# Kernel tuning notes

Hardware: AMD Instinct MI355X
Metric: run time of the kernel (lower is better)

## Reference

```python
import jax, jax.numpy as jnp
import numpy as np
import math

D_MODEL = 1024
NUM_HEADS = 16
MAX_LEN = 2048
B, S = 2, 2048


def setup_inputs() -> dict:
    key = jax.random.key(0)
    ks = jax.random.split(key, 6)
    w_scale = 1.0 / math.sqrt(D_MODEL)  # ~xavier
    return {
        "x": jax.random.normal(ks[0], (B, S, D_MODEL), dtype=jnp.float32),
        "Wq": jax.random.normal(ks[1], (D_MODEL, D_MODEL), dtype=jnp.float32) * w_scale,
        "bq": jnp.zeros((D_MODEL,), dtype=jnp.float32),
        "Wk": jax.random.normal(ks[2], (D_MODEL, D_MODEL), dtype=jnp.float32) * w_scale,
        "bk": jnp.zeros((D_MODEL,), dtype=jnp.float32),
        "Wv": jax.random.normal(ks[3], (D_MODEL, D_MODEL), dtype=jnp.float32) * w_scale,
        "bv": jnp.zeros((D_MODEL,), dtype=jnp.float32),
        "Wo": jax.random.normal(ks[4], (D_MODEL, D_MODEL), dtype=jnp.float32) * w_scale,
        "bo": jnp.zeros((D_MODEL,), dtype=jnp.float32),
        "Er": jax.random.normal(ks[5], (MAX_LEN, D_MODEL // NUM_HEADS), dtype=jnp.float32),
    }


def reference(x, Wq, bq, Wk, bk, Wv, bv, Wo, bo, Er):
    Bsz, Sl, Dm = x.shape
    H = NUM_HEADS
    dqk = Dm // H

    def split_heads(z):
        # [B,S,D] -> [B,H,S,dqk]
        return z.reshape(Bsz, Sl, H, dqk).transpose(0, 2, 1, 3)

    Q = split_heads(x @ Wq.T + bq)
    K = split_heads(x @ Wk.T + bk)
    V = split_heads(x @ Wv.T + bv)

    Er_sl = Er[MAX_LEN - Sl:, :]  # [S, dqk]
    # Faithful to source: contract over d -> [B,H,S], unsqueeze last dim
    QEr = jnp.einsum('bhld,ld->bhl', Q, Er_sl)[..., None]  # [B,H,S,1]
    # skew(): pad left by 1 on last dim, reshape, drop first row
    padded = jnp.pad(QEr, ((0, 0), (0, 0), (0, 0), (1, 0)))  # [B,H,S,2]
    Srel = padded.reshape(Bsz, H, 2, Sl)[:, :, 1:, :]  # [B,H,1,S]

    QK_t = jnp.einsum('bhld,bhmd->bhlm', Q, K)  # [B,H,S,S]
    attn_scores = (QK_t + Srel) / math.sqrt(dqk)

    causal = jnp.tril(jnp.ones((Sl, Sl), dtype=bool))  # [S,S]
    attn_scores = jnp.where(causal[None, None], attn_scores, -jnp.inf)

    attn_probs = jax.nn.softmax(attn_scores, axis=-1)
    attn_out = jnp.einsum('bhlm,bhmd->bhld', attn_probs, V)  # [B,H,S,dqk]
    attn_out = attn_out.transpose(0, 2, 1, 3).reshape(Bsz, Sl, Dm)
    return attn_out @ Wo.T + bo  # dropout omitted (eval mode)
```

## Files before the change

### kernel.cpp

```cpp
#include <hip/hip_runtime.h>
#include <hip/hip_bf16.h>

#define D_MODEL 1024
#define NHEAD 16
#define DH 64
#define BSZ 2
#define SEQ 2048
#define MROWS (BSZ*SEQ)
#define SCL_Q 0.1803368801111204f
#define CHSZ2 16896

typedef __attribute__((ext_vector_type(4))) float f32x4;
typedef __attribute__((ext_vector_type(8))) __bf16 bf16x8;
typedef __attribute__((ext_vector_type(8))) unsigned short u16x8;

__device__ __forceinline__ float b2f(unsigned short u) {
    union { unsigned int i; float f; } v; v.i = ((unsigned int)u) << 16; return v.f;
}
__device__ __forceinline__ unsigned short f2b(float f) {
    union { float f; unsigned int i; } v; v.f = f;
    unsigned int u = v.i;
    u += 0x7fffu + ((u >> 16) & 1u);
    return (unsigned short)(u >> 16);
}

__device__ __forceinline__ char* slotptr(char* wsb, int s) {
    const size_t MB = 1024*1024;
    if (s < 372)  return wsb + 8*MB            + (size_t)s * CHSZ2;
    if (s < 868)  return wsb + 32*MB           + (size_t)(s - 372) * CHSZ2;
    return              wsb + 48*MB + 262144   + (size_t)(s - 868) * CHSZ2;
}

#define GLDS16(gptr, lptr) \
    __builtin_amdgcn_global_load_lds((__attribute__((address_space(1))) void*)(gptr), \
                                     (__attribute__((address_space(3))) void*)(lptr), 16, 0, 0)

__global__ __launch_bounds__(256) void cvt5(
    const float* __restrict__ sx,
    const float* __restrict__ s1, const float* __restrict__ s2,
    const float* __restrict__ s3, const float* __restrict__ s4,
    unsigned short* __restrict__ dx,
    unsigned short* __restrict__ d1, unsigned short* __restrict__ d2,
    unsigned short* __restrict__ d3, unsigned short* __restrict__ d4)
{
    const int seg = blockIdx.y;
    const float* src; unsigned short* dst; int n4;
    if (seg == 0)      { src = sx; dst = dx; n4 = MROWS*D_MODEL/4; }
    else if (seg == 1) { src = s1; dst = d1; n4 = D_MODEL*D_MODEL/4; }
    else if (seg == 2) { src = s2; dst = d2; n4 = D_MODEL*D_MODEL/4; }
    else if (seg == 3) { src = s3; dst = d3; n4 = D_MODEL*D_MODEL/4; }
    else               { src = s4; dst = d4; n4 = D_MODEL*D_MODEL/4; }
    int i = blockIdx.x * 256 + threadIdx.x;
    int stride = gridDim.x * 256;
    for (; i < n4; i += stride) {
        float4 v = ((const float4*)src)[i];
        ushort4 o;
        o.x = f2b(v.x); o.y = f2b(v.y); o.z = f2b(v.z); o.w = f2b(v.w);
        ((ushort4*)dst)[i] = o;
    }
}

__global__ __launch_bounds__(256) void gemm_qkv(
    const unsigned short* __restrict__ X,
    const unsigned short* __restrict__ Wq, const unsigned short* __restrict__ Wk,
    const unsigned short* __restrict__ Wv,
    const float* __restrict__ bq, const float* __restrict__ bk, const float* __restrict__ bv,
    unsigned short* __restrict__ Qo, unsigned short* __restrict__ Ko, unsigned short* __restrict__ Vo)
{
    __shared__ unsigned short lsA[2][128*32];
    __shared__ unsigned short lsB[2][128*32];
    const int tid = threadIdx.x;
    const int z = blockIdx.z;
    const unsigned short* W = (z==0) ? Wq : (z==1) ? Wk : Wv;
    const float* bias = (z==0) ? bq : (z==1) ? bk : bv;
    unsigned short* Out = (z==0) ? Qo : (z==1) ? Ko : Vo;
    const int tM = blockIdx.y * 128;
    const int tN = blockIdx.x * 128;
    const int w = tid >> 6, lane = tid & 63;
    const int wr = w >> 1, wc = w & 1;
    const int lr = lane & 15, lk = lane >> 4;
    const f32x4 fz = {0.f, 0.f, 0.f, 0.f};
    f32x4 acc[4][4];
    #pragma unroll
    for (int m = 0; m < 4; m++)
        #pragma unroll
        for (int n = 0; n < 4; n++) acc[m][n] = fz;

    const int e0 = tid, e1 = 256 + tid;
    const int r0 = e0 >> 2, c0 = ((e0 & 3) ^ (r0 & 3)) * 8;
    const int r1 = e1 >> 2, c1 = ((e1 & 3) ^ (r1 & 3)) * 8;

#define GEMM_STAGE(buf, k0_) do { \
        GLDS16(X + (size_t)(tM + r0) * D_MODEL + (k0_) + c0, &lsA[buf][e0 * 8]); \
        GLDS16(X + (size_t)(tM + r1) * D_MODEL + (k0_) + c1, &lsA[buf][e1 * 8]); \
        GLDS16(W + (size_t)(tN + r0) * D_MODEL + (k0_) + c0, &lsB[buf][e0 * 8]); \
        GLDS16(W + (size_t)(tN + r1) * D_MODEL + (k0_) + c1, &lsB[buf][e1 * 8]); \
    } while (0)

    GEMM_STAGE(0, 0);
    __syncthreads();
    int cur = 0;
    for (int k0 = 0; k0 < D_MODEL; k0 += 32) {
        if (k0 + 32 < D_MODEL) GEMM_STAGE(cur ^ 1, k0 + 32);
        bf16x8 af[4], bfr[4];
        #pragma unroll
        for (int m = 0; m < 4; m++) {
            int row = wr*64 + m*16 + lr;
            af[m] = *(const bf16x8*)&lsA[cur][row*32 + ((lk ^ (row & 3)) * 8)];
        }
        #pragma unroll
        for (int n = 0; n < 4; n++) {
            int row = wc*64 + n*16 + lr;
            bfr[n] = *(const bf16x8*)&lsB[cur][row*32 + ((lk ^ (row & 3)) * 8)];
        }
        #pragma unroll
        for (int m = 0; m < 4; m++)
            #pragma unroll
            for (int n = 0; n < 4; n++)
                acc[m][n] = __builtin_amdgcn_mfma_f32_16x16x32_bf16(af[m], bfr[n], acc[m][n], 0, 0, 0);
        __syncthreads();
        cur ^= 1;
    }
#undef GEMM_STAGE
    const float qscl = (z == 0) ? SCL_Q : 1.0f;
    #pragma unroll
    for (int m = 0; m < 4; m++) {
        int ibase = tM + wr*64 + m*16 + lk*4;
        #pragma unroll
        for (int n = 0; n < 4; n++) {
            int j = tN + wc*64 + n*16 + lr;
            float bj = bias[j];
            int h = j >> 6, d = j & 63;
            #pragma unroll
            for (int r = 0; r < 4; r++) {
                int row = ibase + r;
                int b = row >> 11, s = row & 2047;
                Out[((size_t)(b*NHEAD + h) * SEQ + s) * DH + d] = f2b((acc[m][n][r] + bj) * qscl);
            }
        }
    }
}

__global__ __launch_bounds__(512) void gemm_out(
    const unsigned short* __restrict__ X, const unsigned short* __restrict__ W,
    const float* __restrict__ bias, float* __restrict__ Out)
{
    __shared__ unsigned short lsA[2][128*32];
    __shared__ unsigned short lsB[2][64*32];
    const int tid = threadIdx.x;
    const int tM = blockIdx.y * 128;
    const int tN = blockIdx.x * 64;
    const int w = tid >> 6, lane = tid & 63;
    const int wr = w >> 1, wc = w & 1;
    const int lr = lane & 15, lk = lane >> 4;
    const f32x4 fz = {0.f, 0.f, 0.f, 0.f};
    f32x4 acc[2][2];
    #pragma unroll
    for (int m = 0; m < 2; m++)
        #pragma unroll
        for (int n = 0; n < 2; n++) acc[m][n] = fz;

    const int ra = tid >> 2, ca = ((tid & 3) ^ (ra & 3)) * 8;
    const int eb = tid & 255;
    const int rb = eb >> 2, cb = ((eb & 3) ^ (rb & 3)) * 8;

#define OUT_STAGE(buf, k0_) do { \
        GLDS16(X + (size_t)(tM + ra) * D_MODEL + (k0_) + ca, &lsA[buf][tid * 8]); \
        if (tid < 256) GLDS16(W + (size_t)(tN + rb) * D_MODEL + (k0_) + cb, &lsB[buf][eb * 8]); \
    } while (0)

    OUT_STAGE(0, 0);
    __syncthreads();
    int cur = 0;
    for (int k0 = 0; k0 < D_MODEL; k0 += 32) {
        if (k0 + 32 < D_MODEL) OUT_STAGE(cur ^ 1, k0 + 32);
        bf16x8 af[2], bfr[2];
        #pragma unroll
        for (int m = 0; m < 2; m++) {
            int row = wr*32 + m*16 + lr;
            af[m] = *(const bf16x8*)&lsA[cur][row*32 + ((lk ^ (row & 3)) * 8)];
        }
        #pragma unroll
        for (int n = 0; n < 2; n++) {
            int row = wc*32 + n*16 + lr;
            bfr[n] = *(const bf16x8*)&lsB[cur][row*32 + ((lk ^ (row & 3)) * 8)];
        }
        #pragma unroll
        for (int m = 0; m < 2; m++)
            #pragma unroll
            for (int n = 0; n < 2; n++)
                acc[m][n] = __builtin_amdgcn_mfma_f32_16x16x32_bf16(af[m], bfr[n], acc[m][n], 0, 0, 0);
        __syncthreads();
        cur ^= 1;
    }
#undef OUT_STAGE
    #pragma unroll
    for (int m = 0; m < 2; m++) {
        int ibase = tM + wr*32 + m*16 + lk*4;
        #pragma unroll
        for (int n = 0; n < 2; n++) {
            int j = tN + wc*32 + n*16 + lr;
            float bj = bias[j];
            #pragma unroll
            for (int r = 0; r < 4; r++)
                Out[(size_t)(ibase + r) * D_MODEL + j] = acc[m][n][r] + bj;
        }
    }
}

__global__ __launch_bounds__(256) void vtrans(const unsigned short* __restrict__ V,
                                              unsigned short* __restrict__ Vt) {
    __shared__ unsigned short t[64][80];
    const int bh = blockIdx.y;
    const int s0 = blockIdx.x * 64;
    const int tid = threadIdx.x;
    #pragma unroll
    for (int i = 0; i < 2; i++) {
        int e = i*256 + tid;
        int r = e >> 3, c = e & 7;
        u16x8 v = *(const u16x8*)&V[((size_t)bh * SEQ + s0 + r) * DH + c*8];
        *(u16x8*)&t[r][c*8] = v;
    }
    __syncthreads();
    #pragma unroll
    for (int i = 0; i < 2; i++) {
        int e = i*256 + tid;
        int d = e >> 3, c = e & 7;
        u16x8 o;
        #pragma unroll
        for (int j = 0; j < 8; j++) o[j] = t[c*8 + j][d];
        *(u16x8*)&Vt[((size_t)bh * DH + d) * SEQ + s0 + c*8] = o;
    }
}

__global__ __launch_bounds__(256) void qer_k(const unsigned short* __restrict__ Q,
                                             const float* __restrict__ Er,
                                             float* __restrict__ qer) {
    int gw = blockIdx.x * 4 + (threadIdx.x >> 6);
    int lane = threadIdx.x & 63;
    int bh = gw >> 10;
    int l = 1024 + (gw & 1023);
    float p = b2f(Q[((size_t)bh * SEQ + l) * DH + lane]) * Er[l * DH + lane];
    #pragma unroll
    for (int m = 32; m >= 1; m >>= 1) p += __shfl_xor(p, m, 64);
    if (lane == 0) qer[(size_t)bh * SEQ + l] = p;
}

__global__ __launch_bounds__(256, 3) void attn_k(
    const unsigned short* __restrict__ Q, const unsigned short* __restrict__ Kg,
    const unsigned short* __restrict__ Vt, const float* __restrict__ qer,
    unsigned short* __restrict__ Om, char* __restrict__ wsb)
{
    __shared__ unsigned short lsK[2][64*64];
    __shared__ unsigned short lsV[2][64*64];
    __shared__ unsigned short lsP[128*64];
    const unsigned char jt[40]  = {15,15,15,15,14,14,11,11,11,10, 7, 7, 3,
                                   14,14,13,13,13,13,12,12,10,10, 9, 9, 6, 6,
                                   12,12, 9, 8, 8, 8, 5, 5, 2, 4, 4, 1, 0};
    const unsigned char k0t[40] = { 0, 8,16,24, 0, 8, 0, 8,16, 0, 0, 8, 0,
                                   16,23, 0, 7,14,21, 0, 7, 8,15, 0, 7, 0, 7,
                                   14,20,14, 0, 6,12, 0, 6, 0, 0, 5, 0, 0};
    const unsigned char k1t[40] = { 8,16,24,32, 8,16, 8,16,24, 8, 8,16, 8,
                                   23,30, 7,14,21,28, 7,14,15,22, 7,14, 7,14,
                                   20,26,20, 6,12,18, 6,12, 6, 5,10, 4, 2};
    const unsigned char st40[40]= {32,33,34,35,28,29,17,18,19,14, 6, 7,255,
                                   30,31,24,25,26,27,20,21,15,16,11,12, 4, 5,
                                   22,23,13, 8, 9,10, 2, 3,255, 0, 1,255,255};
    const int id = blockIdx.x;
    const int bh = id & 31;
    const int u = id >> 5;
    const int j = jt[u];
    const int kt0 = k0t[u];
    const int ktN = k1t[u];
    const int sl = st40[u];
    const int b = bh >> 4, h = bh & 15;
    const int tid = threadIdx.x;
    const int w = tid >> 6, lane = tid & 63;
    const int lr = lane & 15, lk = lane >> 4;
    const int q0 = w*32 + lr, q1 = q0 + 16;
    const int qrow0 = j*128 + q0, qrow1 = qrow0 + 16;
    const f32x4 fz = {0.f, 0.f, 0.f, 0.f};

    const unsigned short* Qr0 = Q + ((size_t)bh * SEQ + qrow0) * DH;
    const unsigned short* Qr1 = Q + ((size_t)bh * SEQ + qrow1) * DH;
    bf16x8 bqa0 = *(const bf16x8*)&Qr0[lk*8];
    bf16x8 bqa1 = *(const bf16x8*)&Qr0[32 + lk*8];
    bf16x8 bqb0 = *(const bf16x8*)&Qr1[lk*8];
    bf16x8 bqb1 = *(const bf16x8*)&Qr1[32 + lk*8];

    const int sr0 = tid >> 3,          sc0 = ((tid & 7) ^ (sr0 & 7)) * 8;
    const int sr1 = (256 + tid) >> 3,  sc1 = (((256 + tid) & 7) ^ (sr1 & 7)) * 8;
    const unsigned short* kst0 = Kg + ((size_t)bh * SEQ + kt0*64 + sr0) * DH + sc0;
    const unsigned short* kst1 = Kg + ((size_t)bh * SEQ + kt0*64 + sr1) * DH + sc1;
    const unsigned short* vst0 = Vt + ((size_t)bh * DH + sr0) * SEQ + kt0*64 + sc0;
    const unsigned short* vst1 = Vt + ((size_t)bh * DH + sr1) * SEQ + kt0*64 + sc1;
    const float* qb = qer + (size_t)bh * SEQ + 1024 + kt0*32 + lk*2;

#define ATTN_STAGE(buf) do { \
        GLDS16(kst0, &lsK[buf][tid * 8]);        kst0 += 64*DH; \
        GLDS16(kst1, &lsK[buf][(256+tid) * 8]);  kst1 += 64*DH; \
        GLDS16(vst0, &lsV[buf][tid * 8]);        vst0 += 64; \
        GLDS16(vst1, &lsV[buf][(256+tid) * 8]);  vst1 += 64; \
    } while (0)

    f32x4 o0[4], o1[4];
    #pragma unroll
    for (int df = 0; df < 4; df++) { o0[df] = fz; o1[df] = fz; }
    float lp0 = 0.0f, lp1 = 0.0f;

    ATTN_STAGE(0);
    __syncthreads();
    int cur = 0;

    for (int kt = kt0; kt < ktN; kt++) {
        float2 bv[4];
        #pragma unroll
        for (int kf = 0; kf < 4; kf++) bv[kf] = *(const float2*)(qb + kf*8);
        qb += 32;
        if (kt + 1 < ktN) ATTN_STAGE(cur ^ 1);
        float st[4][4], su[4][4];
        __builtin_amdgcn_s_setprio(1);
        #pragma unroll
        for (int kf = 0; kf < 4; kf++) {
            int row = kf*16 + lr;
            bf16x8 a0 = *(const bf16x8*)&lsK[cur][row*64 + ((lk ^ (row & 7)) * 8)];
            bf16x8 a1 = *(const bf16x8*)&lsK[cur][row*64 + (((4 + lk) ^ (row & 7)) * 8)];
            f32x4 zv = fz, yv = fz;
            zv = __builtin_amdgcn_mfma_f32_16x16x32_bf16(a0, bqa0, zv, 0, 0, 0);
            zv = __builtin_amdgcn_mfma_f32_16x16x32_bf16(a1, bqa1, zv, 0, 0, 0);
            yv = __builtin_amdgcn_mfma_f32_16x16x32_bf16(a0, bqb0, yv, 0, 0, 0);
            yv = __builtin_amdgcn_mfma_f32_16x16x32_bf16(a1, bqb1, yv, 0, 0, 0);
            st[kf][0] = zv[0];
            st[kf][1] = zv[1] + bv[kf].x;
            st[kf][2] = zv[2];
            st[kf][3] = zv[3] + bv[kf].y;
            su[kf][0] = yv[0];
            su[kf][1] = yv[1] + bv[kf].x;
            su[kf][2] = yv[2];
            su[kf][3] = yv[3] + bv[kf].y;
        }
        __builtin_amdgcn_s_setprio(0);
        if (kt >= 2*j) {
            #pragma unroll
            for (int kf = 0; kf < 4; kf++) {
                int kg0 = kt*64 + kf*16 + lk*4;
                #pragma unroll
                for (int r = 0; r < 4; r++) {
                    if (kg0 + r > qrow0) st[kf][r] = -3.0e38f;
                    if (kg0 + r > qrow1) su[kf][r] = -3.0e38f;
                }
            }
        }
        #pragma unroll
        for (int kf = 0; kf < 4; kf++) {
            float p0 = exp2f(st[kf][0]);
            float p1 = exp2f(st[kf][1]);
            float p2 = exp2f(st[kf][2]);
            float p3 = exp2f(st[kf][3]);
            lp0 += (p0 + p1) + (p2 + p3);
            union { __hip_bfloat162 h2[2]; unsigned long long u; } pk;
            pk.h2[0] = __float22bfloat162_rn(float2{p0, p1});
            pk.h2[1] = __float22bfloat162_rn(float2{p2, p3});
            *(unsigned long long*)&lsP[q0*64 + ((((kf<<2)|lk) ^ ((lr&7)<<1))<<2)] = pk.u;
            float s0 = exp2f(su[kf][0]);
            float s1 = exp2f(su[kf][1]);
            float s2 = exp2f(su[kf][2]);
            float s3 = exp2f(su[kf][3]);
            lp1 += (s0 + s1) + (s2 + s3);
            pk.h2[0] = __float22bfloat162_rn(float2{s0, s1});
            pk.h2[1] = __float22bfloat162_rn(float2{s2, s3});
            *(unsigned long long*)&lsP[q1*64 + ((((kf<<2)|lk) ^ ((lr&7)<<1))<<2)] = pk.u;
        }
        bf16x8 pa0 = *(const bf16x8*)&lsP[q0*64 + ((lk ^ (lr&7))<<3)];
        bf16x8 pa1 = *(const bf16x8*)&lsP[q0*64 + (((4+lk) ^ (lr&7))<<3)];
        bf16x8 pb0 = *(const bf16x8*)&lsP[q1*64 + ((lk ^ (lr&7))<<3)];
        bf16x8 pb1 = *(const bf16x8*)&lsP[q1*64 + (((4+lk) ^ (lr&7))<<3)];
        __builtin_amdgcn_s_setprio(1);
        #pragma unroll
        for (int df = 0; df < 4; df++) {
            int row = df*16 + lr;
            bf16x8 v0 = *(const bf16x8*)&lsV[cur][row*64 + ((lk ^ (row & 7)) * 8)];
            bf16x8 v1 = *(const bf16x8*)&lsV[cur][row*64 + (((4 + lk) ^ (row & 7)) * 8)];
            o0[df] = __builtin_amdgcn_mfma_f32_16x16x32_bf16(v0, pa0, o0[df], 0, 0, 0);
            o0[df] = __builtin_amdgcn_mfma_f32_16x16x32_bf16(v1, pa1, o0[df], 0, 0, 0);
            o1[df] = __builtin_amdgcn_mfma_f32_16x16x32_bf16(v0, pb0, o1[df], 0, 0, 0);
            o1[df] = __builtin_amdgcn_mfma_f32_16x16x32_bf16(v1, pb1, o1[df], 0, 0, 0);
        }
        __builtin_amdgcn_s_setprio(0);
        __syncthreads();
        cur ^= 1;
    }
#undef ATTN_STAGE
    float l0 = lp0 + __shfl_xor(lp0, 16, 64);
    l0 += __shfl_xor(l0, 32, 64);
    float l1 = lp1 + __shfl_xor(lp1, 16, 64);
    l1 += __shfl_xor(l1, 32, 64);
    if (sl != 255) {
        char* cb = slotptr(wsb, bh*36 + sl);
        unsigned short* ob = (unsigned short*)cb;
        #pragma unroll
        for (int df = 0; df < 4; df++) {
            ushort4 ov;
            ov.x = f2b(o0[df][0]); ov.y = f2b(o0[df][1]);
            ov.z = f2b(o0[df][2]); ov.w = f2b(o0[df][3]);
            *(ushort4*)&ob[q0*64 + df*16 + lk*4] = ov;
            ov.x = f2b(o1[df][0]); ov.y = f2b(o1[df][1]);
            ov.z = f2b(o1[df][2]); ov.w = f2b(o1[df][3]);
            *(ushort4*)&ob[q1*64 + df*16 + lk*4] = ov;
        }
        float* lv = (float*)(cb + 16384);
        if (lk == 0) { lv[q0] = l0; lv[q1] = l1; }
    } else {
        float inv0 = 1.0f / l0, inv1 = 1.0f / l1;
        #pragma unroll
        for (int df = 0; df < 4; df++) {
            ushort4 ov;
            ov.x = f2b(o0[df][0] * inv0);
            ov.y = f2b(o0[df][1] * inv0);
            ov.z = f2b(o0[df][2] * inv0);
            ov.w = f2b(o0[df][3] * inv0);
            *(ushort4*)&Om[((size_t)(b * SEQ + qrow0)) * D_MODEL + h*64 + df*16 + lk*4] = ov;
            ov.x = f2b(o1[df][0] * inv1);
            ov.y = f2b(o1[df][1] * inv1);
            ov.z = f2b(o1[df][2] * inv1);
            ov.w = f2b(o1[df][3] * inv1);
            *(ushort4*)&Om[((size_t)(b * SEQ + qrow1)) * D_MODEL + h*64 + df*16 + lk*4] = ov;
        }
    }
}

__global__ __launch_bounds__(256) void attn_merge(char* __restrict__ wsb,
                                                  unsigned short* __restrict__ Om)
{
    const unsigned char offt[12] = {0,2,4,6,8,11,14,17,20,24,28,32};
    const unsigned char nct[12]  = {2,2,2,2,3,3,3,3,4,4,4,4};
    const int bh = blockIdx.x & 31, jj = blockIdx.x >> 5;
    const int b = bh >> 4, h = bh & 15, j = 4 + jj;
    const int nc = nct[jj];
    const int base = bh*36 + offt[jj];
    const int t = threadIdx.x;
    const int q = t >> 1, dh = (t & 1) * 32;
    float acc[32];
    #pragma unroll
    for (int i = 0; i < 32; i++) acc[i] = 0.f;
    float lsum = 0.f;
    for (int c = 0; c < nc; c++) {
        const char* cb = slotptr(wsb, base + c);
        const unsigned short* ob = (const unsigned short*)cb;
        const float* lv = (const float*)(cb + 16384);
        lsum += lv[q];
        #pragma unroll
        for (int i = 0; i < 4; i++) {
            u16x8 a = *(const u16x8*)&ob[q*64 + dh + i*8];
            #pragma unroll
            for (int r = 0; r < 8; r++) acc[i*8 + r] += b2f(a[r]);
        }
    }
    float inv = 1.0f / lsum;
    unsigned short* dst = Om + ((size_t)(b*SEQ + j*128 + q)) * D_MODEL + h*64 + dh;
    #pragma unroll
    for (int i = 0; i < 4; i++) {
        u16x8 ov;
        #pragma unroll
        for (int r = 0; r < 8; r++) ov[r] = f2b(acc[i*8 + r] * inv);
        *(u16x8*)&dst[i*8] = ov;
    }
}

extern "C" void kernel_launch(void* const* d_in, const int* in_sizes, int n_in,
                              void* d_out, int out_size, void* d_ws, size_t ws_size,
                              hipStream_t stream) {
    const float* x  = (const float*)d_in[0];
    const float* Wq = (const float*)d_in[1];
    const float* bq = (const float*)d_in[2];
    const float* Wk = (const float*)d_in[3];
    const float* bk = (const float*)d_in[4];
    const float* Wv = (const float*)d_in[5];
    const float* bv = (const float*)d_in[6];
    const float* Wo = (const float*)d_in[7];
    const float* bo = (const float*)d_in[8];
    const float* Er = (const float*)d_in[9];

    char* ws = (char*)d_ws;
    const size_t MB = 1024*1024;
    unsigned short* xb  = (unsigned short*)(ws);
    unsigned short* Wqb = (unsigned short*)(ws + 8*MB);
    unsigned short* Wkb = (unsigned short*)(ws + 10*MB);
    unsigned short* Wvb = (unsigned short*)(ws + 12*MB);
    unsigned short* Wob = (unsigned short*)(ws + 14*MB);
    unsigned short* Qb  = (unsigned short*)(ws + 16*MB);
    unsigned short* Kb  = (unsigned short*)(ws + 24*MB);
    unsigned short* Vb  = (unsigned short*)(ws + 32*MB);
    unsigned short* Vtb = (unsigned short*)(ws + 40*MB);
    float* qer          = (float*)(ws + 48*MB);

    cvt5<<<dim3(1024, 5), 256, 0, stream>>>(x, Wq, Wk, Wv, Wo, xb, Wqb, Wkb, Wvb, Wob);

    gemm_qkv<<<dim3(8, 32, 3), 256, 0, stream>>>(xb, Wqb, Wkb, Wvb, bq, bk, bv, Qb, Kb, Vb);
    vtrans<<<dim3(32, 32), 256, 0, stream>>>(Vb, Vtb);
    qer_k<<<8192, 256, 0, stream>>>(Qb, Er, qer);
    attn_k<<<1280, 256, 0, stream>>>(Qb, Kb, Vtb, qer, xb, ws);
    attn_merge<<<384, 256, 0, stream>>>(ws, xb);
    gemm_out<<<dim3(16, 32), 512, 0, stream>>>(xb, Wob, bo, (float*)d_out);
}
```

Baseline: 123.4 us.

## Double attention query tile to 256 rows with 512-thread blocks

The attention kernel now processes 256 query rows per block using 8 waves instead of 128 rows with 4 waves. Each K/V tile staged into LDS is therefore shared by twice as many queries, and each thread issues half as many loads per stage. The split-K work schedule, the workspace slot layout and the merge kernel are rebuilt for 8 query tiles per head. The cost is coarser load balancing (640 blocks instead of 1280), a larger LDS footprint per block, and a longer causal-masked tail on diagonal tiles.

```diff
diff --git a/kernel.cpp b/kernel.cpp
--- a/kernel.cpp
+++ b/kernel.cpp
@@ -8,7 +8,7 @@
 #define SEQ 2048
 #define MROWS (BSZ*SEQ)
 #define SCL_Q 0.1803368801111204f
-#define CHSZ2 16896
+#define CHSZ2 33792
 
 typedef __attribute__((ext_vector_type(4))) float f32x4;
 typedef __attribute__((ext_vector_type(8))) __bf16 bf16x8;
@@ -26,9 +26,9 @@
 
 __device__ __forceinline__ char* slotptr(char* wsb, int s) {
     const size_t MB = 1024*1024;
-    if (s < 372)  return wsb + 8*MB            + (size_t)s * CHSZ2;
-    if (s < 868)  return wsb + 32*MB           + (size_t)(s - 372) * CHSZ2;
-    return              wsb + 48*MB + 262144   + (size_t)(s - 868) * CHSZ2;
+    if (s < 186)  return wsb + 8*MB            + (size_t)s * CHSZ2;
+    if (s < 434)  return wsb + 32*MB           + (size_t)(s - 186) * CHSZ2;
+    return              wsb + 48*MB + 262144   + (size_t)(s - 434) * CHSZ2;
 }
 
 #define GLDS16(gptr, lptr) \
@@ -246,39 +246,31 @@
     if (lane == 0) qer[(size_t)bh * SEQ + l] = p;
 }
 
-__global__ __launch_bounds__(256, 3) void attn_k(
+__global__ __launch_bounds__(512, 4) void attn_k(
     const unsigned short* __restrict__ Q, const unsigned short* __restrict__ Kg,
     const unsigned short* __restrict__ Vt, const float* __restrict__ qer,
     unsigned short* __restrict__ Om, char* __restrict__ wsb)
 {
     __shared__ unsigned short lsK[2][64*64];
     __shared__ unsigned short lsV[2][64*64];
-    __shared__ unsigned short lsP[128*64];
-    const unsigned char jt[40]  = {15,15,15,15,14,14,11,11,11,10, 7, 7, 3,
-                                   14,14,13,13,13,13,12,12,10,10, 9, 9, 6, 6,
-                                   12,12, 9, 8, 8, 8, 5, 5, 2, 4, 4, 1, 0};
-    const unsigned char k0t[40] = { 0, 8,16,24, 0, 8, 0, 8,16, 0, 0, 8, 0,
-                                   16,23, 0, 7,14,21, 0, 7, 8,15, 0, 7, 0, 7,
-                                   14,20,14, 0, 6,12, 0, 6, 0, 0, 5, 0, 0};
-    const unsigned char k1t[40] = { 8,16,24,32, 8,16, 8,16,24, 8, 8,16, 8,
-                                   23,30, 7,14,21,28, 7,14,15,22, 7,14, 7,14,
-                                   20,26,20, 6,12,18, 6,12, 6, 5,10, 4, 2};
-    const unsigned char st40[40]= {32,33,34,35,28,29,17,18,19,14, 6, 7,255,
-                                   30,31,24,25,26,27,20,21,15,16,11,12, 4, 5,
-                                   22,23,13, 8, 9,10, 2, 3,255, 0, 1,255,255};
+    __shared__ unsigned short lsP[256*64];
+    const unsigned char jt[20]  = {7,7,7,7, 5,5,5, 3,3, 1, 6,6,6,6, 4,4, 4, 2,2, 0};
+    const unsigned char k0t[20] = {0,8,16,24, 0,8,16, 0,8, 0, 0,7,14,21, 0,7, 14, 0,6, 0};
+    const unsigned char k1t[20] = {8,16,24,32, 8,16,24, 8,16, 8, 7,14,21,28, 7,14, 20, 6,12, 4};
+    const unsigned char st20[20]= {14,15,16,17, 7,8,9, 2,3, 255, 10,11,12,13, 4,5, 6, 0,1, 255};
     const int id = blockIdx.x;
     const int bh = id & 31;
     const int u = id >> 5;
     const int j = jt[u];
     const int kt0 = k0t[u];
     const int ktN = k1t[u];
-    const int sl = st40[u];
+    const int sl = st20[u];
     const int b = bh >> 4, h = bh & 15;
     const int tid = threadIdx.x;
     const int w = tid >> 6, lane = tid & 63;
     const int lr = lane & 15, lk = lane >> 4;
     const int q0 = w*32 + lr, q1 = q0 + 16;
-    const int qrow0 = j*128 + q0, qrow1 = qrow0 + 16;
+    const int qrow0 = j*256 + q0, qrow1 = qrow0 + 16;
     const f32x4 fz = {0.f, 0.f, 0.f, 0.f};
 
     const unsigned short* Qr0 = Q + ((size_t)bh * SEQ + qrow0) * DH;
@@ -288,19 +280,14 @@
     bf16x8 bqb0 = *(const bf16x8*)&Qr1[lk*8];
     bf16x8 bqb1 = *(const bf16x8*)&Qr1[32 + lk*8];
 
-    const int sr0 = tid >> 3,          sc0 = ((tid & 7) ^ (sr0 & 7)) * 8;
-    const int sr1 = (256 + tid) >> 3,  sc1 = (((256 + tid) & 7) ^ (sr1 & 7)) * 8;
-    const unsigned short* kst0 = Kg + ((size_t)bh * SEQ + kt0*64 + sr0) * DH + sc0;
-    const unsigned short* kst1 = Kg + ((size_t)bh * SEQ + kt0*64 + sr1) * DH + sc1;
-    const unsigned short* vst0 = Vt + ((size_t)bh * DH + sr0) * SEQ + kt0*64 + sc0;
-    const unsigned short* vst1 = Vt + ((size_t)bh * DH + sr1) * SEQ + kt0*64 + sc1;
+    const int sr = tid >> 3, sc = ((tid & 7) ^ (sr & 7)) * 8;
+    const unsigned short* kst = Kg + ((size_t)bh * SEQ + kt0*64 + sr) * DH + sc;
+    const unsigned short* vst = Vt + ((size_t)bh * DH + sr) * SEQ + kt0*64 + sc;
     const float* qb = qer + (size_t)bh * SEQ + 1024 + kt0*32 + lk*2;
 
 #define ATTN_STAGE(buf) do { \
-        GLDS16(kst0, &lsK[buf][tid * 8]);        kst0 += 64*DH; \
-        GLDS16(kst1, &lsK[buf][(256+tid) * 8]);  kst1 += 64*DH; \
-        GLDS16(vst0, &lsV[buf][tid * 8]);        vst0 += 64; \
-        GLDS16(vst1, &lsV[buf][(256+tid) * 8]);  vst1 += 64; \
+        GLDS16(kst, &lsK[buf][tid * 8]); kst += 64*DH; \
+        GLDS16(vst, &lsV[buf][tid * 8]); vst += 64; \
     } while (0)
 
     f32x4 o0[4], o1[4];
@@ -340,7 +327,7 @@
             su[kf][3] = yv[3] + bv[kf].y;
         }
         __builtin_amdgcn_s_setprio(0);
-        if (kt >= 2*j) {
+        if (kt >= 4*j) {
             #pragma unroll
             for (int kf = 0; kf < 4; kf++) {
                 int kg0 = kt*64 + kf*16 + lk*4;
@@ -396,7 +383,7 @@
     float l1 = lp1 + __shfl_xor(lp1, 16, 64);
     l1 += __shfl_xor(l1, 32, 64);
     if (sl != 255) {
-        char* cb = slotptr(wsb, bh*36 + sl);
+        char* cb = slotptr(wsb, bh*18 + sl);
         unsigned short* ob = (unsigned short*)cb;
         #pragma unroll
         for (int df = 0; df < 4; df++) {
@@ -408,7 +395,7 @@
             ov.z = f2b(o1[df][2]); ov.w = f2b(o1[df][3]);
             *(ushort4*)&ob[q1*64 + df*16 + lk*4] = ov;
         }
-        float* lv = (float*)(cb + 16384);
+        float* lv = (float*)(cb + 32768);
         if (lk == 0) { lv[q0] = l0; lv[q1] = l1; }
     } else {
         float inv0 = 1.0f / l0, inv1 = 1.0f / l1;
@@ -429,15 +416,15 @@
     }
 }
 
-__global__ __launch_bounds__(256) void attn_merge(char* __restrict__ wsb,
+__global__ __launch_bounds__(512) void attn_merge(char* __restrict__ wsb,
                                                   unsigned short* __restrict__ Om)
 {
-    const unsigned char offt[12] = {0,2,4,6,8,11,14,17,20,24,28,32};
-    const unsigned char nct[12]  = {2,2,2,2,3,3,3,3,4,4,4,4};
+    const unsigned char offt[6] = {0,2,4,7,10,14};
+    const unsigned char nct[6]  = {2,2,3,3,4,4};
     const int bh = blockIdx.x & 31, jj = blockIdx.x >> 5;
-    const int b = bh >> 4, h = bh & 15, j = 4 + jj;
+    const int b = bh >> 4, h = bh & 15, j = 2 + jj;
     const int nc = nct[jj];
-    const int base = bh*36 + offt[jj];
+    const int base = bh*18 + offt[jj];
     const int t = threadIdx.x;
     const int q = t >> 1, dh = (t & 1) * 32;
     float acc[32];
@@ -447,7 +434,7 @@
     for (int c = 0; c < nc; c++) {
         const char* cb = slotptr(wsb, base + c);
         const unsigned short* ob = (const unsigned short*)cb;
-        const float* lv = (const float*)(cb + 16384);
+        const float* lv = (const float*)(cb + 32768);
         lsum += lv[q];
         #pragma unroll
         for (int i = 0; i < 4; i++) {
@@ -457,7 +444,7 @@
         }
     }
     float inv = 1.0f / lsum;
-    unsigned short* dst = Om + ((size_t)(b*SEQ + j*128 + q)) * D_MODEL + h*64 + dh;
+    unsigned short* dst = Om + ((size_t)(b*SEQ + j*256 + q)) * D_MODEL + h*64 + dh;
     #pragma unroll
     for (int i = 0; i < 4; i++) {
         u16x8 ov;
@@ -499,7 +486,7 @@
     gemm_qkv<<<dim3(8, 32, 3), 256, 0, stream>>>(xb, Wqb, Wkb, Wvb, bq, bk, bv, Qb, Kb, Vb);
     vtrans<<<dim3(32, 32), 256, 0, stream>>>(Vb, Vtb);
     qer_k<<<8192, 256, 0, stream>>>(Qb, Er, qer);
-    attn_k<<<1280, 256, 0, stream>>>(Qb, Kb, Vtb, qer, xb, ws);
-    attn_merge<<<384, 256, 0, stream>>>(ws, xb);
+    attn_k<<<640, 512, 0, stream>>>(Qb, Kb, Vtb, qer, xb, ws);
+    attn_merge<<<192, 512, 0, stream>>>(ws, xb);
     gemm_out<<<dim3(16, 32), 512, 0, stream>>>(xb, Wob, bo, (float*)d_out);
 }
```

New measurement: 151.4 us. +22.7%, slower.
